# Performance work log

Hardware: AMD Instinct MI355X
Metric: run time of the kernel (lower is better)

Reference implementation:

```python
import jax, jax.numpy as jnp
import numpy as np

SOFTCAP = 50.0
EPS = 1e-6
N_HEADS, D_HEAD = 16, 64


def _rms(x, w):
    return x * jax.lax.rsqrt(jnp.mean(x * x, axis=-1, keepdims=True) + EPS) * w


def _rope(x, cos, sin):
    # Faithful to source: apply_rope uses x.size(1) as the position axis, but is
    # called on (B, H, T, Dh) tensors, so positions are indexed by HEAD index.
    n = x.shape[1]
    x1, x2 = x[..., 0::2], x[..., 1::2]
    c = cos[:n][None, :, None, :]
    s = sin[:n][None, :, None, :]
    return jnp.stack([x1 * c - x2 * s, x1 * s + x2 * c], axis=-1).reshape(x.shape)


def setup_inputs() -> dict:
    key = jax.random.key(0)
    ks = jax.random.split(key, 12)
    L, D, H, Dh, Dff, V, B, T = 6, 1024, N_HEADS, D_HEAD, 4096, 32000, 1, 1024
    r = lambda k, shape: jax.random.normal(k, shape, dtype=jnp.float32) * 0.02
    return {
        'x': jax.random.randint(ks[0], (B, T), 0, V, dtype=jnp.int32),
        'embed': r(ks[1], (V, D)),
        'ln1': jnp.ones((L, D), jnp.float32),
        'Wq': r(ks[2], (L, H * Dh, D)),
        'Wk': r(ks[3], (L, H * Dh, D)),
        'Wv': r(ks[4], (L, H * Dh, D)),
        'Wo': r(ks[5], (L, D, H * Dh)),
        'qn': jnp.ones((L, Dh), jnp.float32),
        'kn': jnp.ones((L, Dh), jnp.float32),
        'ln2': jnp.ones((L, D), jnp.float32),
        'Wg': r(ks[6], (L, Dff, D)),
        'Wu': r(ks[7], (L, Dff, D)),
        'Wd': r(ks[8], (L, D, Dff)),
        'ln_out': jnp.ones((D,), jnp.float32),
    }


def reference(x, embed, ln1, Wq, Wk, Wv, Wo, qn, kn, ln2, Wg, Wu, Wd, ln_out):
    B, T = x.shape
    H, Dh = N_HEADS, D_HEAD
    scale = Dh ** -0.5
    # RoPE tables (theta=10000)
    freqs = 1.0 / (10000.0 ** (jnp.arange(0, Dh, 2, dtype=jnp.float32) / Dh))
    ang = jnp.arange(T, dtype=jnp.float32)[:, None] * freqs[None, :]
    cos, sin = jnp.cos(ang), jnp.sin(ang)
    mask = jnp.triu(jnp.ones((T, T), dtype=bool), k=1)  # True above diagonal

    h = embed[x]  # (B, T, D)

    def block(h, p):
        l1, wq, wk, wv, wo, qnw, knw, l2, wg, wu, wd = p
        hn = _rms(h, l1)
        q = (hn @ wq.T).reshape(B, T, H, Dh).transpose(0, 2, 1, 3)  # (B,H,T,Dh)
        k = (hn @ wk.T).reshape(B, T, H, Dh).transpose(0, 2, 1, 3)
        v = (hn @ wv.T).reshape(B, T, H, Dh).transpose(0, 2, 1, 3)
        q = _rope(_rms(q, qnw), cos, sin)
        k = _rope(_rms(k, knw), cos, sin)
        scores = jnp.einsum('bhtd,bhsd->bhts', q, k) * scale
        scores = SOFTCAP * jnp.tanh(scores / SOFTCAP)
        scores = jnp.where(mask[None, None], -jnp.inf, scores)
        attn = jax.nn.softmax(scores, axis=-1)
        o = jnp.einsum('bhts,bhsd->bhtd', attn, v)
        o = o.transpose(0, 2, 1, 3).reshape(B, T, H * Dh)
        h = h + o @ wo.T
        hn2 = _rms(h, l2)
        h = h + (jax.nn.silu(hn2 @ wg.T) * (hn2 @ wu.T)) @ wd.T
        return h, None

    h, _ = jax.lax.scan(block, h, (ln1, Wq, Wk, Wv, Wo, qn, kn, ln2, Wg, Wu, Wd))
    # tied embed/head
    logits = _rms(h, ln_out) @ embed.T  # (B, T, V)
    return logits
```

## Files before the change

kernel.cpp:

```cpp
#include <hip/hip_runtime.h>
#include <math.h>
#include <type_traits>

typedef __bf16 bf16_t;
typedef bf16_t bf16x4 __attribute__((ext_vector_type(4)));
typedef bf16_t bf16x8 __attribute__((ext_vector_type(8)));
typedef float  f32x4  __attribute__((ext_vector_type(4)));

#define RMS_EPS 1e-6f

enum { EP_STORE = 0, EP_RESID = 1, EP_SPLIT = 2, EP_SILU = 3, EP_QKV = 4 };

template<int V> using IC = std::integral_constant<int, V>;

static __device__ __forceinline__ f32x4 mfma16(bf16x8 a, bf16x8 b, f32x4 c) {
    return __builtin_amdgcn_mfma_f32_16x16x32_bf16(a, b, c, 0, 0, 0);
}

#define GLDS(gp, lp) __builtin_amdgcn_global_load_lds( \
    (const __attribute__((address_space(1))) void*)(gp), \
    (__attribute__((address_space(3))) void*)(lp), 16, 0, 0)

template<int N> static __device__ __forceinline__ void vmwait() {
    if constexpr (N == 0)      asm volatile("s_waitcnt vmcnt(0)" ::: "memory");
    else if constexpr (N == 2) asm volatile("s_waitcnt vmcnt(2)" ::: "memory");
    else if constexpr (N == 3) asm volatile("s_waitcnt vmcnt(3)" ::: "memory");
    else if constexpr (N == 4) asm volatile("s_waitcnt vmcnt(4)" ::: "memory");
    else if constexpr (N == 6) asm volatile("s_waitcnt vmcnt(6)" ::: "memory");
    else if constexpr (N == 8) asm volatile("s_waitcnt vmcnt(8)" ::: "memory");
    __builtin_amdgcn_sched_barrier(0);
}
static __device__ __forceinline__ void bar() { __builtin_amdgcn_s_barrier(); }
static __device__ __forceinline__ void lgkm0() {
    asm volatile("s_waitcnt lgkmcnt(0)" ::: "memory");
    __builtin_amdgcn_sched_barrier(0);
}

template<int BM, int BN, int WR, int WC, int PLANES, int EPIL, int MINW, int DEPTH>
__global__ __launch_bounds__(WR * WC * 64, MINW)
void gemm_bf16(const bf16_t* __restrict__ Ah, const bf16_t* __restrict__ Al,
               const bf16_t* __restrict__ Bh,
               float* __restrict__ Cf, bf16_t* __restrict__ Ch, bf16_t* __restrict__ Cl,
               int K, int lda, int ldb, int ldc, long long sC,
               const float* __restrict__ qnw, const float* __restrict__ knw)
{
    constexpr int ASZ = BM * 32, BSZ = BN * 32;
    constexpr int NW = WR * WC;
    constexpr int NLD = (BM / 16 * (PLANES >= 2 ? 2 : 1) + BN / 16) / NW;
    __shared__ __align__(16) bf16_t sAh[DEPTH][ASZ], sBh[DEPTH][BSZ];
    __shared__ __align__(16) bf16_t sAl[PLANES >= 2 ? DEPTH : 1][PLANES >= 2 ? ASZ : 8];

    const int gx = gridDim.x;
    int id = blockIdx.x + gx * blockIdx.y;
    if (gridDim.z == 1) {
        int nwg = gx * gridDim.y;
        int q = nwg >> 3, r = nwg & 7;
        int xcd = id & 7, ix = id >> 3;
        id = (xcd < r ? xcd * (q + 1) : r * (q + 1) + (xcd - r) * q) + ix;
    }
    const int bm = id % gx, bn = id / gx;
    const int row0 = bm * BM, col0 = bn * BN;

    const size_t kofs = (size_t)blockIdx.z * K;
    Ah += kofs;  Bh += kofs;
    if constexpr (PLANES >= 2) Al += kofs;

    const int tid = threadIdx.x, lane = tid & 63, wave = tid >> 6;
    const int lr = lane & 15, lg = lane >> 4;
    constexpr int WM = BM / WR, WN = BN / WC, MF = WM / 16, NF = WN / 16;
    const int wr = wave / WC, wc = wave % WC;

    f32x4 acc[MF][NF];
    #pragma unroll
    for (int m = 0; m < MF; ++m)
        #pragma unroll
        for (int n = 0; n < NF; ++n) acc[m][n] = (f32x4){0.f, 0.f, 0.f, 0.f};

    auto stage = [&](int k0, int p) {
        #pragma unroll
        for (int i = wave; i < BM / 16; i += NW) {
            int s = i * 64 + lane, rr = s >> 2, c = s & 3;
            size_t go = (size_t)(row0 + rr) * lda + k0 + ((c ^ ((rr >> 1) & 3)) << 3);
            GLDS(Ah + go, &sAh[p][i * 512]);
            if constexpr (PLANES >= 2) GLDS(Al + go, &sAl[p][i * 512]);
        }
        #pragma unroll
        for (int i = wave; i < BN / 16; i += NW) {
            int s = i * 64 + lane, rr = s >> 2, c = s & 3;
            size_t go = (size_t)(col0 + rr) * ldb + k0 + ((c ^ ((rr >> 1) & 3)) << 3);
            GLDS(Bh + go, &sBh[p][i * 512]);
        }
    };

    auto compute = [&](int p) {
        bf16x8 ahf[MF], alf[MF], bhf[NF];
        #pragma unroll
        for (int m = 0; m < MF; ++m) {
            int rr = wr * WM + m * 16 + lr;
            int by = rr * 64 + ((lg ^ ((rr >> 1) & 3)) << 4);
            ahf[m] = *(const bf16x8*)((const char*)&sAh[p][0] + by);
            if constexpr (PLANES >= 2)
                alf[m] = *(const bf16x8*)((const char*)&sAl[p][0] + by);
        }
        #pragma unroll
        for (int n = 0; n < NF; ++n) {
            int rr = wc * WN + n * 16 + lr;
            int by = rr * 64 + ((lg ^ ((rr >> 1) & 3)) << 4);
            bhf[n] = *(const bf16x8*)((const char*)&sBh[p][0] + by);
        }
        #pragma unroll
        for (int m = 0; m < MF; ++m)
            #pragma unroll
            for (int n = 0; n < NF; ++n) {
                acc[m][n] = mfma16(ahf[m], bhf[n], acc[m][n]);
                if constexpr (PLANES >= 2)
                    acc[m][n] = mfma16(alf[m], bhf[n], acc[m][n]);
            }
    };

    if constexpr (DEPTH == 3) {
        const int NC = K >> 5;
        stage(0, 0);
        stage(32, 1);
        for (int j = 0; j + 2 < NC; ++j) {
            stage(32 * (j + 2), (j + 2) % 3);
            vmwait<2 * NLD>(); bar();
            compute(j % 3);
            bar();
        }
        vmwait<NLD>(); bar();
        compute((K >> 5) >= 2 ? ((K >> 5) - 2) % 3 : 0);
        vmwait<0>(); bar();
        compute(((K >> 5) - 1) % 3);
    } else {
        stage(0, 0);
        int k0 = 32;
        for (; k0 + 32 < K; k0 += 64) {
            stage(k0, 1);
            vmwait<NLD>(); bar();
            compute(0);
            bar();
            stage(k0 + 32, 0);
            vmwait<NLD>(); bar();
            compute(1);
            bar();
        }
        stage(k0, 1);
        vmwait<NLD>(); bar();
        compute(0);
        bar();
        vmwait<0>(); bar();
        compute(1);
    }

    if constexpr (EPIL == EP_QKV) {
        const int colbase = col0 + wc * WN;
        const int typ = colbase >> 10;
        if (typ < 2) {
            const float* nw = (typ == 0) ? qnw : knw;
            const int hh = (colbase - typ * 1024) >> 6;
            constexpr float kLogF = -0.41524101186092029f;
            #pragma unroll
            for (int m = 0; m < MF; ++m)
                #pragma unroll
                for (int r = 0; r < 4; ++r) {
                    int grow = row0 + wr * WM + m * 16 + lg * 4 + r;
                    float ss = 0.f;
                    #pragma unroll
                    for (int n = 0; n < NF; ++n) {
                        float v = acc[m][n][r];
                        ss += v * v;
                    }
                    ss += __shfl_xor(ss, 1, 64);
                    ss += __shfl_xor(ss, 2, 64);
                    ss += __shfl_xor(ss, 4, 64);
                    ss += __shfl_xor(ss, 8, 64);
                    float inv = rsqrtf(ss * (1.0f / 64.0f) + RMS_EPS);
                    #pragma unroll
                    for (int n = 0; n < NF; ++n) {
                        int i = n * 16 + lr;
                        float x = acc[m][n][r] * inv * nw[i];
                        float p = __shfl_xor(x, 1, 64);
                        float f = exp2f((float)(i >> 1) * kLogF);
                        float ang = (float)hh * f;
                        float cs = cosf(ang), sn = sinf(ang);
                        float o = (lr & 1) ? (p * sn + x * cs) : (x * cs - p * sn);
                        Ch[(size_t)grow * ldc + colbase + i] = (bf16_t)o;
                    }
                }
        } else {
            bf16_t* vTh_ = Cl;
            bf16_t* vTl_ = (bf16_t*)Cf;
            const int vcb = colbase - 2048;
            #pragma unroll
            for (int m = 0; m < MF; ++m)
                #pragma unroll
                for (int n = 0; n < NF; ++n) {
                    int vc = vcb + n * 16 + lr;
                    int grow0 = row0 + wr * WM + m * 16 + lg * 4;
                    bf16x4 hv, lv;
                    #pragma unroll
                    for (int r = 0; r < 4; ++r) {
                        float v = acc[m][n][r];
                        bf16_t hb = (bf16_t)v;
                        hv[r] = hb;
                        lv[r] = (bf16_t)(v - (float)hb);
                    }
                    *(bf16x4*)&vTh_[(size_t)vc * 1024 + grow0] = hv;
                    *(bf16x4*)&vTl_[(size_t)vc * 1024 + grow0] = lv;
                }
        }
        return;
    }

    #pragma unroll
    for (int m = 0; m < MF; ++m)
        #pragma unroll
        for (int n = 0; n < NF; ++n)
            #pragma unroll
            for (int r = 0; r < 4; ++r) {
                int grow = row0 + wr * WM + m * 16 + lg * 4 + r;
                int gcol = col0 + wc * WN + n * 16 + lr;
                float v = acc[m][n][r];
                size_t off = (size_t)blockIdx.z * sC + (size_t)grow * ldc + gcol;
                if constexpr (EPIL == EP_STORE) {
                    Cf[off] = v;
                } else if constexpr (EPIL == EP_RESID) {
                    Cf[off] += v;
                } else if constexpr (EPIL == EP_SPLIT) {
                    bf16_t hb = (bf16_t)v;
                    Ch[off] = hb;
                    Cl[off] = (bf16_t)(v - (float)hb);
                }
            }
}

__global__ __launch_bounds__(512, 4)
void gemm_gu_pack(const bf16_t* __restrict__ Ah, const bf16_t* __restrict__ Bh,
                  bf16_t* __restrict__ Ch,
                  const float* wq, const float* wk, const float* wv,
                  const float* wo, const float* wg, const float* wu,
                  const float* wd, bf16_t* wAd, bf16_t* wGUd, bf16_t* wdd,
                  const float* __restrict__ embed, bf16_t* __restrict__ eh,
                  int es, int ee)
{
    constexpr int lda = 1024, ldb = 1024, ldc = 4096, K = 1024;
    const int tid = threadIdx.x;

    if (blockIdx.z == 2) {
        int base = ((int)blockIdx.y * 8 + (int)blockIdx.x) * 512 + tid;
        for (int j = 0; j < 11; ++j) {
            int u = es + j * 131072 + base;
            if (u < ee) {
                f32x4 v = ((const f32x4*)embed)[u];
                bf16x4 hv;
                #pragma unroll
                for (int q2 = 0; q2 < 4; ++q2) hv[q2] = (bf16_t)v[q2];
                ((bf16x4*)eh)[u] = hv;
            }
        }
        return;
    }

    if (blockIdx.z == 1) {
        if (!wq) return;
        int base = ((int)blockIdx.y * 8 + (int)blockIdx.x) * 512 + tid;
        #pragma unroll 4
        for (int j = 0; j < 32; ++j) {
            int v = j * 131072 + base;
            f32x4 val;
            bf16_t* dst;
            size_t doff;
            if (v < (1 << 20)) {
                int b = v >> 8, col = v & 255;
                const float* src = b < 1024 ? wq : b < 2048 ? wk : b < 3072 ? wv : wo;
                val = ((const f32x4*)src)[(size_t)(b & 1023) * 256 + col];
                dst = wAd; doff = (size_t)b * 256 + col;
            } else if (v < 3 * (1 << 20)) {
                int u = v - (1 << 20);
                int bb = u >> 8, col = u & 255;
                int row = bb < 4096 ? 2 * bb : 2 * (bb - 4096) + 1;
                const float* src = bb < 4096 ? wg : wu;
                val = ((const f32x4*)src)[(size_t)(bb & 4095) * 256 + col];
                dst = wGUd; doff = (size_t)row * 256 + col;
            } else {
                int u = v - 3 * (1 << 20);
                val = ((const f32x4*)wd)[u];
                dst = wdd; doff = (size_t)u;
            }
            bf16x4 hv;
            #pragma unroll
            for (int q2 = 0; q2 < 4; ++q2) hv[q2] = (bf16_t)val[q2];
            ((bf16x4*)dst)[doff] = hv;
        }
        return;
    }

    __shared__ __align__(16) bf16_t sA[3][128 * 32], sB[3][256 * 32];

    int id = blockIdx.x + 8 * blockIdx.y;
    {
        int q = 256 >> 3;
        int xcd = id & 7, ix = id >> 3;
        id = xcd * q + ix;
    }
    const int bm = id % 8, bn = id / 8;
    const int row0 = bm * 128, col0 = bn * 256;

    const int lane = tid & 63, wave = tid >> 6;
    const int lr = lane & 15, lg = lane >> 4;
    const int wr = wave >> 2, wc = wave & 3;

    f32x4 acc[4][4];
    #pragma unroll
    for (int m = 0; m < 4; ++m)
        #pragma unroll
        for (int n = 0; n < 4; ++n) acc[m][n] = (f32x4){0.f, 0.f, 0.f, 0.f};

    auto stage = [&](int k0, int p) {
        {
            int i = wave;
            int s = i * 64 + lane, rr = s >> 2, c = s & 3;
            size_t go = (size_t)(row0 + rr) * lda + k0 + ((c ^ ((rr >> 1) & 3)) << 3);
            GLDS(Ah + go, &sA[p][i * 512]);
        }
        #pragma unroll
        for (int i = wave; i < 16; i += 8) {
            int s = i * 64 + lane, rr = s >> 2, c = s & 3;
            size_t go = (size_t)(col0 + rr) * ldb + k0 + ((c ^ ((rr >> 1) & 3)) << 3);
            GLDS(Bh + go, &sB[p][i * 512]);
        }
    };

    auto compute = [&](int p) {
        bf16x8 af[4], bf4[4];
        #pragma unroll
        for (int m = 0; m < 4; ++m) {
            int rr = wr * 64 + m * 16 + lr;
            int by = rr * 64 + ((lg ^ ((rr >> 1) & 3)) << 4);
            af[m] = *(const bf16x8*)((const char*)&sA[p][0] + by);
        }
        #pragma unroll
        for (int n = 0; n < 4; ++n) {
            int rr = wc * 64 + n * 16 + lr;
            int by = rr * 64 + ((lg ^ ((rr >> 1) & 3)) << 4);
            bf4[n] = *(const bf16x8*)((const char*)&sB[p][0] + by);
        }
        #pragma unroll
        for (int m = 0; m < 4; ++m)
            #pragma unroll
            for (int n = 0; n < 4; ++n)
                acc[m][n] = mfma16(af[m], bf4[n], acc[m][n]);
    };

    const int NC = K >> 5;
    stage(0, 0);
    stage(32, 1);
    for (int j = 0; j + 2 < NC; ++j) {
        stage(32 * (j + 2), (j + 2) % 3);
        vmwait<6>(); bar();
        compute(j % 3);
        bar();
    }
    vmwait<3>(); bar();
    compute((NC - 2) % 3);
    vmwait<0>(); bar();
    compute((NC - 1) % 3);

    #pragma unroll
    for (int m = 0; m < 4; ++m)
        #pragma unroll
        for (int n = 0; n < 4; ++n)
            #pragma unroll
            for (int r = 0; r < 4; ++r) {
                int grow = row0 + wr * 64 + m * 16 + lg * 4 + r;
                int gcol = col0 + wc * 64 + n * 16 + lr;
                float v = acc[m][n][r];
                float pv = __shfl_xor(v, 1, 64);
                if (!(lr & 1)) {
                    float s = (v / (1.0f + __expf(-v))) * pv;
                    Ch[(size_t)grow * ldc + (gcol >> 1)] = (bf16_t)s;
                }
            }
}

__global__ __launch_bounds__(512, 2)
void gemm_logits8(const bf16_t* __restrict__ Ah, const bf16_t* __restrict__ Bh,
                  float* __restrict__ Cf)
{
    constexpr int lda = 1024, ldb = 1024, ldc = 32000;
    constexpr int NT = 16;
    __shared__ __align__(16) bf16_t sA[2][2][256 * 32];
    __shared__ __align__(16) bf16_t sB[2][2][256 * 32];

    const int gx = gridDim.x;
    int id = blockIdx.x + gx * blockIdx.y;
    {
        int nwg = gx * gridDim.y;
        int q = nwg >> 3, r = nwg & 7;
        int xcd = id & 7, ix = id >> 3;
        id = (xcd < r ? xcd * (q + 1) : r * (q + 1) + (xcd - r) * q) + ix;
    }
    const int bm = id % gx, bn = id / gx;
    const int row0 = bm * 256, col0 = bn * 256;

    const int tid = threadIdx.x, lane = tid & 63, wave = tid >> 6;
    const int lr = lane & 15, lg = lane >> 4;
    const int wr = wave >> 2, wc = wave & 3;

    f32x4 acc[8][4];
    #pragma unroll
    for (int m = 0; m < 8; ++m)
        #pragma unroll
        for (int n = 0; n < 4; ++n) acc[m][n] = (f32x4){0.f, 0.f, 0.f, 0.f};

    auto stageA = [&](int chunk, int buf, int ks) {
        int k0 = chunk * 32;
        #pragma unroll
        for (int i = wave; i < 16; i += 8) {
            int s = i * 64 + lane, rr = s >> 2, c = s & 3;
            size_t go = (size_t)(row0 + rr) * lda + k0 + ((c ^ ((rr >> 1) & 3)) << 3);
            GLDS(Ah + go, &sA[buf][ks][i * 512]);
        }
    };
    auto stageB = [&](int chunk, int buf, int ks) {
        int k0 = chunk * 32;
        #pragma unroll
        for (int i = wave; i < 16; i += 8) {
            int s = i * 64 + lane, rr = s >> 2, c = s & 3;
            size_t go = (size_t)(col0 + rr) * ldb + k0 + ((c ^ ((rr >> 1) & 3)) << 3);
            GLDS(Bh + go, &sB[buf][ks][i * 512]);
        }
    };

    auto phase = [&](int t, auto ksc) {
        constexpr int ks = decltype(ksc)::value;
        const int buf = t & 1;
        bf16x8 af[8], bf4[4];
        #pragma unroll
        for (int m = 0; m < 8; ++m) {
            int rr = wr * 128 + m * 16 + lr;
            int by = rr * 64 + ((lg ^ ((rr >> 1) & 3)) << 4);
            af[m] = *(const bf16x8*)((const char*)&sA[buf][ks][0] + by);
        }
        #pragma unroll
        for (int n = 0; n < 4; ++n) {
            int rr = wc * 64 + n * 16 + lr;
            int by = rr * 64 + ((lg ^ ((rr >> 1) & 3)) << 4);
            bf4[n] = *(const bf16x8*)((const char*)&sB[buf][ks][0] + by);
        }
        if constexpr (ks == 0) {
            if (t + 1 < NT) {
                stageA(2 * (t + 1) + 1, (t + 1) & 1, 1);
                stageB(2 * (t + 1) + 1, (t + 1) & 1, 1);
                vmwait<8>();
            } else {
                vmwait<0>();
            }
        } else {
            if (t + 2 < NT) {
                stageA(2 * (t + 2), t & 1, 0);
                stageB(2 * (t + 2), t & 1, 0);
                vmwait<8>();
            } else if (t + 1 < NT) {
                vmwait<4>();
            } else {
                vmwait<0>();
            }
        }
        bar();
        lgkm0();
        __builtin_amdgcn_s_setprio(1);
        #pragma unroll
        for (int m = 0; m < 8; ++m)
            #pragma unroll
            for (int n = 0; n < 4; ++n)
                acc[m][n] = mfma16(af[m], bf4[n], acc[m][n]);
        __builtin_amdgcn_s_setprio(0);
        bar();
    };

    stageA(0, 0, 0); stageB(0, 0, 0);
    stageA(1, 0, 1); stageB(1, 0, 1);
    stageA(2, 1, 0); stageB(2, 1, 0);
    vmwait<8>(); bar();

    for (int t = 0; t < NT; ++t) {
        phase(t, IC<0>{});
        phase(t, IC<1>{});
    }

    #pragma unroll
    for (int m = 0; m < 8; ++m)
        #pragma unroll
        for (int n = 0; n < 4; ++n)
            #pragma unroll
            for (int r = 0; r < 4; ++r) {
                int grow = row0 + wr * 128 + m * 16 + lg * 4 + r;
                int gcol = col0 + wc * 64 + n * 16 + lr;
                Cf[(size_t)grow * ldc + gcol] = acc[m][n][r];
            }
}

static __device__ __forceinline__ void wsplit_body(
    int b2, int tid,
    const float* wq, const float* wk, const float* wv, const float* wo,
    const float* wg, const float* wu, const float* wd,
    bf16_t* wAh, bf16_t* wGUh, bf16_t* wdh)
{
    #pragma unroll
    for (int k = 0; k < 4; ++k) {
        int b = b2 * 4 + k;
        const float* src;
        bf16_t* dst;
        size_t so, doff;
        if (b < 4096) {
            src = b < 1024 ? wq : b < 2048 ? wk : b < 3072 ? wv : wo;
            so = (size_t)(b & 1023) * 256 + tid;
            doff = (size_t)b * 256 + tid;
            dst = wAh;
        } else if (b < 12288) {
            int bb = b - 4096;
            int row = bb < 4096 ? 2 * bb : 2 * (bb - 4096) + 1;
            src = bb < 4096 ? wg : wu;
            so = (size_t)(bb & 4095) * 256 + tid;
            doff = (size_t)row * 256 + tid;
            dst = wGUh;
        } else {
            src = wd;
            so = (size_t)(b - 12288) * 256 + tid;
            doff = so;
            dst = wdh;
        }
        f32x4 v = ((const f32x4*)src)[so];
        bf16x4 hv;
        #pragma unroll
        for (int j = 0; j < 4; ++j) hv[j] = (bf16_t)v[j];
        ((bf16x4*)dst)[doff] = hv;
    }
}

__global__ __launch_bounds__(256)
void reduce_rms(const float* __restrict__ p, float* __restrict__ h,
                const float* __restrict__ w, bf16_t* __restrict__ outh)
{
    int blk = blockIdx.x, tid = threadIdx.x;
    size_t i = (size_t)blk * 256 + tid;
    const size_t S = (1024 * 1024) / 4;
    f32x4 a = ((const f32x4*)p)[i];
    f32x4 b = ((const f32x4*)p)[i + S];
    f32x4 c = ((const f32x4*)p)[i + 2 * S];
    f32x4 d = ((const f32x4*)p)[i + 3 * S];
    f32x4 hv = ((const f32x4*)h)[i];
    #pragma unroll
    for (int j = 0; j < 4; ++j) hv[j] += (a[j] + b[j]) + (c[j] + d[j]);
    ((f32x4*)h)[i] = hv;

    float ss = hv[0]*hv[0] + hv[1]*hv[1] + hv[2]*hv[2] + hv[3]*hv[3];
    #pragma unroll
    for (int m = 1; m < 64; m <<= 1) ss += __shfl_xor(ss, m, 64);
    __shared__ float red[4];
    if ((tid & 63) == 0) red[tid >> 6] = ss;
    __syncthreads();
    float tot = red[0] + red[1] + red[2] + red[3];
    float inv = rsqrtf(tot * (1.0f / 1024.0f) + RMS_EPS);
    f32x4 wt4 = *(const f32x4*)(w + tid * 4);
    bf16x4 hv4;
    #pragma unroll
    for (int j = 0; j < 4; ++j) hv4[j] = (bf16_t)(hv[j] * inv * wt4[j]);
    ((bf16x4*)outh)[i] = hv4;
}

__global__ __launch_bounds__(256)
void gather_rms_wsplit(const int* __restrict__ ids, const float* __restrict__ embed,
                       const float* __restrict__ w, float* __restrict__ h,
                       bf16_t* __restrict__ outh,
                       const float* wq, const float* wk, const float* wv,
                       const float* wo, const float* wg, const float* wu,
                       const float* wd, bf16_t* wAh, bf16_t* wGUh, bf16_t* wdh)
{
    int blk = blockIdx.x, tid = threadIdx.x;
    if (blk >= 1024) {
        wsplit_body(blk - 1024, tid, wq, wk, wv, wo, wg, wu, wd, wAh, wGUh, wdh);
        return;
    }
    int row = ids[blk];
    f32x4 v = ((const f32x4*)(embed + (size_t)row * 1024))[tid];
    ((f32x4*)(h + (size_t)blk * 1024))[tid] = v;

    float ss = v[0]*v[0] + v[1]*v[1] + v[2]*v[2] + v[3]*v[3];
    #pragma unroll
    for (int m = 1; m < 64; m <<= 1) ss += __shfl_xor(ss, m, 64);
    __shared__ float red[4];
    if ((tid & 63) == 0) red[tid >> 6] = ss;
    __syncthreads();
    float tot = red[0] + red[1] + red[2] + red[3];
    float inv = rsqrtf(tot * (1.0f / 1024.0f) + RMS_EPS);
    f32x4 wt4 = *(const f32x4*)(w + tid * 4);
    bf16x4 hv;
    #pragma unroll
    for (int j = 0; j < 4; ++j) hv[j] = (bf16_t)(v[j] * inv * wt4[j]);
    ((bf16x4*)outh)[(size_t)blk * 256 + tid] = hv;
}

__global__ __launch_bounds__(128, 2)
void flash_attn(const bf16_t* __restrict__ qkvh,
                const bf16_t* __restrict__ vTh, const bf16_t* __restrict__ vTl,
                bf16_t* __restrict__ oh)
{
    __shared__ __align__(16) bf16_t sQ[32*64], sK[64*64], sVh[64*64], sVl[64*64];
    __shared__ __align__(16) bf16_t sPh[32*64], sPl[32*64];

    const int q0 = blockIdx.x * 32;
    const int hh = blockIdx.y;
    const int tid = threadIdx.x, lane = tid & 63, w = tid >> 6;
    const int lr = lane & 15, lg = lane >> 4;

    #pragma unroll
    for (int ii = 0; ii < 2; ++ii) {
        int r0 = w * 16 + ii * 8;
        int r  = r0 + (lane >> 3);
        int i  = lane & 7;
        GLDS(qkvh + (size_t)(q0 + r) * 3072 + hh * 64 + ((i ^ (r & 7)) << 3),
             sQ + r0 * 64);
    }
    __syncthreads();

    bf16x8 qa[2];
    #pragma unroll
    for (int ks = 0; ks < 2; ++ks) {
        int r = w * 16 + lr;
        qa[ks] = *(const bf16x8*)((const char*)sQ + r * 128 +
                                  ((((ks << 2) | lg) ^ (r & 7)) << 4));
    }

    f32x4 o_acc[4];
    #pragma unroll
    for (int n = 0; n < 4; ++n) o_acc[n] = (f32x4){0.f, 0.f, 0.f, 0.f};
    float m_run[4] = {-1e30f, -1e30f, -1e30f, -1e30f};
    float l_run[4] = {0.f, 0.f, 0.f, 0.f};

    const int ntiles = ((q0 + 31) >> 6) + 1;
    for (int t = 0; t < ntiles; ++t) {
        const int kv0 = t * 64;
        #pragma unroll
        for (int ii = 0; ii < 4; ++ii) {
            int r0 = w * 32 + ii * 8;
            int r  = r0 + (lane >> 3);
            int i  = lane & 7;
            GLDS(qkvh + (size_t)(kv0 + r) * 3072 + 1024 + hh * 64 + ((i ^ (r & 7)) << 3),
                 sK + r0 * 64);
            GLDS(vTh + (size_t)(hh * 64 + r) * 1024 + kv0 + ((i ^ (r & 7)) << 3),
                 sVh + r0 * 64);
            GLDS(vTl + (size_t)(hh * 64 + r) * 1024 + kv0 + ((i ^ (r & 7)) << 3),
                 sVl + r0 * 64);
        }
        __syncthreads();

        f32x4 s_acc[4];
        #pragma unroll
        for (int n = 0; n < 4; ++n) s_acc[n] = (f32x4){0.f, 0.f, 0.f, 0.f};
        #pragma unroll
        for (int ks = 0; ks < 2; ++ks)
            #pragma unroll
            for (int n = 0; n < 4; ++n) {
                int r = n * 16 + lr;
                bf16x8 kb = *(const bf16x8*)((const char*)sK + r * 128 +
                                             ((((ks << 2) | lg) ^ (r & 7)) << 4));
                s_acc[n] = mfma16(qa[ks], kb, s_acc[n]);
            }

        #pragma unroll
        for (int j = 0; j < 4; ++j) {
            int qr = q0 + w * 16 + lg * 4 + j;
            float p[4];
            float mx = -1e30f;
            #pragma unroll
            for (int n = 0; n < 4; ++n) {
                float sx = s_acc[n][j] * (0.125f * 0.02f);
                float v = 50.f * (1.f - 2.f / (1.f + __expf(2.f * sx)));
                int key = kv0 + n * 16 + lr;
                if (key > qr) v = -1e30f;
                p[n] = v;
                mx = fmaxf(mx, v);
            }
            #pragma unroll
            for (int m = 1; m < 16; m <<= 1) mx = fmaxf(mx, __shfl_xor(mx, m, 64));
            float mn = fmaxf(m_run[j], mx);
            float ef = __expf(m_run[j] - mn);
            m_run[j] = mn;
            float rs = 0.f;
            #pragma unroll
            for (int n = 0; n < 4; ++n) {
                float e = __expf(p[n] - mn);
                p[n] = e;
                rs += e;
            }
            #pragma unroll
            for (int m = 1; m < 16; m <<= 1) rs += __shfl_xor(rs, m, 64);
            l_run[j] = l_run[j] * ef + rs;
            #pragma unroll
            for (int n = 0; n < 4; ++n) o_acc[n][j] *= ef;
            int r = w * 16 + lg * 4 + j;
            #pragma unroll
            for (int n = 0; n < 4; ++n) {
                int c = n * 16 + lr;
                int byo = r * 128 + ((((c >> 3) ^ (r & 7)) << 4)) + ((c & 7) << 1);
                bf16_t hb = (bf16_t)p[n];
                *(bf16_t*)((char*)sPh + byo) = hb;
                *(bf16_t*)((char*)sPl + byo) = (bf16_t)(p[n] - (float)hb);
            }
        }

        #pragma unroll
        for (int ks = 0; ks < 2; ++ks) {
            int pr = w * 16 + lr;
            int pby = pr * 128 + ((((ks << 2) | lg) ^ (pr & 7)) << 4);
            bf16x8 pa  = *(const bf16x8*)((const char*)sPh + pby);
            bf16x8 pl_ = *(const bf16x8*)((const char*)sPl + pby);
            #pragma unroll
            for (int n = 0; n < 4; ++n) {
                int vr = n * 16 + lr;
                int vby = vr * 128 + ((((ks << 2) | lg) ^ (vr & 7)) << 4);
                bf16x8 vhf = *(const bf16x8*)((const char*)sVh + vby);
                bf16x8 vlf = *(const bf16x8*)((const char*)sVl + vby);
                o_acc[n] = mfma16(pa,  vhf, o_acc[n]);
                o_acc[n] = mfma16(pl_, vhf, o_acc[n]);
                o_acc[n] = mfma16(pa,  vlf, o_acc[n]);
            }
        }
        __syncthreads();
    }

    #pragma unroll
    for (int j = 0; j < 4; ++j) {
        float inv = 1.0f / l_run[j];
        int qr = q0 + w * 16 + lg * 4 + j;
        #pragma unroll
        for (int n = 0; n < 4; ++n) {
            size_t off = (size_t)qr * 1024 + hh * 64 + n * 16 + lr;
            oh[off] = (bf16_t)(o_acc[n][j] * inv);
        }
    }
}

__global__ __launch_bounds__(256)
void rmsnorm_split(const float* __restrict__ in, const float* __restrict__ w,
                   bf16_t* __restrict__ outh)
{
    int row = blockIdx.x, tid = threadIdx.x;
    f32x4 v = *(const f32x4*)(in + (size_t)row * 1024 + tid * 4);
    float ss = v[0]*v[0] + v[1]*v[1] + v[2]*v[2] + v[3]*v[3];
    #pragma unroll
    for (int m = 1; m < 64; m <<= 1) ss += __shfl_xor(ss, m, 64);
    __shared__ float red[4];
    if ((tid & 63) == 0) red[tid >> 6] = ss;
    __syncthreads();
    float tot = red[0] + red[1] + red[2] + red[3];
    float inv = rsqrtf(tot * (1.0f / 1024.0f) + RMS_EPS);
    f32x4 wt4 = *(const f32x4*)(w + tid * 4);
    bf16x4 hv;
    #pragma unroll
    for (int j = 0; j < 4; ++j) hv[j] = (bf16_t)(v[j] * inv * wt4[j]);
    ((bf16x4*)outh)[(size_t)row * 256 + tid] = hv;
}

extern "C" void kernel_launch(void* const* d_in, const int* in_sizes, int n_in,
                              void* d_out, int out_size, void* d_ws, size_t ws_size,
                              hipStream_t stream)
{
    (void)in_sizes; (void)n_in; (void)out_size; (void)ws_size;
    const int*   x_ids = (const int*)  d_in[0];
    const float* embed = (const float*)d_in[1];
    const float* ln1   = (const float*)d_in[2];
    const float* Wq    = (const float*)d_in[3];
    const float* Wk    = (const float*)d_in[4];
    const float* Wv    = (const float*)d_in[5];
    const float* Wo    = (const float*)d_in[6];
    const float* qn    = (const float*)d_in[7];
    const float* kn    = (const float*)d_in[8];
    const float* ln2   = (const float*)d_in[9];
    const float* Wg    = (const float*)d_in[10];
    const float* Wu    = (const float*)d_in[11];
    const float* Wd    = (const float*)d_in[12];
    const float* lnout = (const float*)d_in[13];
    float* out = (float*)d_out;

    char* ws = (char*)d_ws;
    const size_t MB = 1 << 20;
    float*  h    = (float*) (ws +   0 * MB);
    bf16_t* hnh  = (bf16_t*)(ws +   4 * MB);
    bf16_t* qkvh = (bf16_t*)(ws +   8 * MB);
    bf16_t* vTh  = (bf16_t*)(ws +  20 * MB);
    bf16_t* vTl  = (bf16_t*)(ws +  22 * MB);
    bf16_t* oh   = (bf16_t*)(ws +  24 * MB);
    bf16_t* wA[2]  = {(bf16_t*)(ws +  28 * MB), (bf16_t*)(ws +  84 * MB)};
    bf16_t* wGU[2] = {(bf16_t*)(ws +  36 * MB), (bf16_t*)(ws +  92 * MB)};
    bf16_t* wD[2]  = {(bf16_t*)(ws +  52 * MB), (bf16_t*)(ws + 108 * MB)};
    bf16_t* silh = (bf16_t*)(ws +  60 * MB);
    float*  wdp  = (float*) (ws +  68 * MB);
    bf16_t* eh   = (bf16_t*)(ws + 116 * MB);

    const long long M1 = 1024 * 1024;
    const int ETOT = 8192000;
    const int ESL  = 1365334;

    gather_rms_wsplit<<<5120, 256, 0, stream>>>(
        x_ids, embed, ln1, h, hnh,
        Wq, Wk, Wv, Wo, Wg, Wu, Wd, wA[0], wGU[0], wD[0]);

    for (int l = 0; l < 6; ++l) {
        const int s = l & 1, nx = s ^ 1;

        gemm_bf16<64,128,2,2,1,EP_QKV,4,3><<<dim3(16,24),256,0,stream>>>(
            hnh, nullptr, wA[s], (float*)vTl, qkvh, vTh, 1024, 1024, 1024, 3072, 0,
            qn + l * 64, kn + l * 64);

        flash_attn<<<dim3(32,16), 128, 0, stream>>>(qkvh, vTh, vTl, oh);

        gemm_bf16<64,64,2,2,1,EP_RESID,4,3><<<dim3(16,16),256,0,stream>>>(
            oh, nullptr, wA[s] + 3 * M1, h, nullptr, nullptr, 1024, 1024, 1024, 1024, 0,
            nullptr, nullptr);

        rmsnorm_split<<<1024, 256, 0, stream>>>(h, ln2 + l * 1024, hnh);

        int es = l * ESL, ee = (l + 1) * ESL < ETOT ? (l + 1) * ESL : ETOT;
        gemm_gu_pack<<<dim3(8,32,3), 512, 0, stream>>>(
            hnh, wGU[s], silh,
            l < 5 ? Wq + (size_t)(l+1) * M1 : nullptr,
            l < 5 ? Wk + (size_t)(l+1) * M1 : nullptr,
            l < 5 ? Wv + (size_t)(l+1) * M1 : nullptr,
            l < 5 ? Wo + (size_t)(l+1) * M1 : nullptr,
            l < 5 ? Wg + (size_t)(l+1) * 4 * M1 : nullptr,
            l < 5 ? Wu + (size_t)(l+1) * 4 * M1 : nullptr,
            l < 5 ? Wd + (size_t)(l+1) * 4 * M1 : nullptr,
            wA[nx], wGU[nx], wD[nx],
            embed, eh, es, ee);

        gemm_bf16<128,128,2,2,1,EP_STORE,4,3><<<dim3(8,8,4),256,0,stream>>>(
            silh, nullptr, wD[s], wdp, nullptr, nullptr, 1024, 4096, 4096, 1024, M1,
            nullptr, nullptr);

        const float* wnext = (l < 5) ? (ln1 + (l + 1) * 1024) : lnout;
        reduce_rms<<<1024, 256, 0, stream>>>(wdp, h, wnext, hnh);
    }

    gemm_logits8<<<dim3(4,125), 512, 0, stream>>>(hnh, eh, out);
}
```

Before: 1.095 ms.

## Double-buffer K/V tiles in flash attention and precompute RoPE tables

Flash attention now stages the next K/V tile into a second LDS buffer while the current tile is being computed. Partial vmcnt waits let the compute overlap with the global-to-LDS loads instead of stalling on a full sync every tile. Separately, the RoPE cos/sin values are computed once into small tables by an extra block of the setup kernel, so the QKV GEMM epilogue reads them instead of evaluating exp2/cos/sin per element. This costs double the K/V LDS footprint, which may reduce occupancy, plus a small table read per element.

```diff
diff --git a/kernel.cpp b/kernel.cpp
--- a/kernel.cpp
+++ b/kernel.cpp
@@ -22,12 +22,13 @@
     (__attribute__((address_space(3))) void*)(lp), 16, 0, 0)
 
 template<int N> static __device__ __forceinline__ void vmwait() {
-    if constexpr (N == 0)      asm volatile("s_waitcnt vmcnt(0)" ::: "memory");
-    else if constexpr (N == 2) asm volatile("s_waitcnt vmcnt(2)" ::: "memory");
-    else if constexpr (N == 3) asm volatile("s_waitcnt vmcnt(3)" ::: "memory");
-    else if constexpr (N == 4) asm volatile("s_waitcnt vmcnt(4)" ::: "memory");
-    else if constexpr (N == 6) asm volatile("s_waitcnt vmcnt(6)" ::: "memory");
-    else if constexpr (N == 8) asm volatile("s_waitcnt vmcnt(8)" ::: "memory");
+    if constexpr (N == 0)       asm volatile("s_waitcnt vmcnt(0)" ::: "memory");
+    else if constexpr (N == 2)  asm volatile("s_waitcnt vmcnt(2)" ::: "memory");
+    else if constexpr (N == 3)  asm volatile("s_waitcnt vmcnt(3)" ::: "memory");
+    else if constexpr (N == 4)  asm volatile("s_waitcnt vmcnt(4)" ::: "memory");
+    else if constexpr (N == 6)  asm volatile("s_waitcnt vmcnt(6)" ::: "memory");
+    else if constexpr (N == 8)  asm volatile("s_waitcnt vmcnt(8)" ::: "memory");
+    else if constexpr (N == 12) asm volatile("s_waitcnt vmcnt(12)" ::: "memory");
     __builtin_amdgcn_sched_barrier(0);
 }
 static __device__ __forceinline__ void bar() { __builtin_amdgcn_s_barrier(); }
@@ -42,7 +43,8 @@
                const bf16_t* __restrict__ Bh,
                float* __restrict__ Cf, bf16_t* __restrict__ Ch, bf16_t* __restrict__ Cl,
                int K, int lda, int ldb, int ldc, long long sC,
-               const float* __restrict__ qnw, const float* __restrict__ knw)
+               const float* __restrict__ qnw, const float* __restrict__ knw,
+               const float* __restrict__ ctab, const float* __restrict__ stab)
 {
     constexpr int ASZ = BM * 32, BSZ = BN * 32;
     constexpr int NW = WR * WC;
@@ -159,7 +161,6 @@
         if (typ < 2) {
             const float* nw = (typ == 0) ? qnw : knw;
             const int hh = (colbase - typ * 1024) >> 6;
-            constexpr float kLogF = -0.41524101186092029f;
             #pragma unroll
             for (int m = 0; m < MF; ++m)
                 #pragma unroll
@@ -181,9 +182,8 @@
                         int i = n * 16 + lr;
                         float x = acc[m][n][r] * inv * nw[i];
                         float p = __shfl_xor(x, 1, 64);
-                        float f = exp2f((float)(i >> 1) * kLogF);
-                        float ang = (float)hh * f;
-                        float cs = cosf(ang), sn = sinf(ang);
+                        float cs = ctab[(hh << 5) + (i >> 1)];
+                        float sn = stab[(hh << 5) + (i >> 1)];
                         float o = (lr & 1) ? (p * sn + x * cs) : (x * cs - p * sn);
                         Ch[(size_t)grow * ldc + colbase + i] = (bf16_t)o;
                     }
@@ -577,9 +577,21 @@
                        bf16_t* __restrict__ outh,
                        const float* wq, const float* wk, const float* wv,
                        const float* wo, const float* wg, const float* wu,
-                       const float* wd, bf16_t* wAh, bf16_t* wGUh, bf16_t* wdh)
+                       const float* wd, bf16_t* wAh, bf16_t* wGUh, bf16_t* wdh,
+                       float* __restrict__ ctab, float* __restrict__ stab)
 {
     int blk = blockIdx.x, tid = threadIdx.x;
+    if (blk == 5120) {
+        constexpr float kLogF = -0.41524101186092029f;
+        for (int e = tid; e < 512; e += 256) {
+            int hh = e >> 5, p0 = e & 31;
+            float f = exp2f((float)p0 * kLogF);
+            float ang = (float)hh * f;
+            ctab[e] = cosf(ang);
+            stab[e] = sinf(ang);
+        }
+        return;
+    }
     if (blk >= 1024) {
         wsplit_body(blk - 1024, tid, wq, wk, wv, wo, wg, wu, wd, wAh, wGUh, wdh);
         return;
@@ -608,7 +620,8 @@
                 const bf16_t* __restrict__ vTh, const bf16_t* __restrict__ vTl,
                 bf16_t* __restrict__ oh)
 {
-    __shared__ __align__(16) bf16_t sQ[32*64], sK[64*64], sVh[64*64], sVl[64*64];
+    __shared__ __align__(16) bf16_t sQ[32*64];
+    __shared__ __align__(16) bf16_t sK[2][64*64], sVh[2][64*64], sVl[2][64*64];
     __shared__ __align__(16) bf16_t sPh[32*64], sPl[32*64];
 
     const int q0 = blockIdx.x * 32;
@@ -624,24 +637,8 @@
         GLDS(qkvh + (size_t)(q0 + r) * 3072 + hh * 64 + ((i ^ (r & 7)) << 3),
              sQ + r0 * 64);
     }
-    __syncthreads();
-
-    bf16x8 qa[2];
-    #pragma unroll
-    for (int ks = 0; ks < 2; ++ks) {
-        int r = w * 16 + lr;
-        qa[ks] = *(const bf16x8*)((const char*)sQ + r * 128 +
-                                  ((((ks << 2) | lg) ^ (r & 7)) << 4));
-    }
-
-    f32x4 o_acc[4];
-    #pragma unroll
-    for (int n = 0; n < 4; ++n) o_acc[n] = (f32x4){0.f, 0.f, 0.f, 0.f};
-    float m_run[4] = {-1e30f, -1e30f, -1e30f, -1e30f};
-    float l_run[4] = {0.f, 0.f, 0.f, 0.f};
-
-    const int ntiles = ((q0 + 31) >> 6) + 1;
-    for (int t = 0; t < ntiles; ++t) {
+
+    auto stageKV = [&](int t, int buf) {
         const int kv0 = t * 64;
         #pragma unroll
         for (int ii = 0; ii < 4; ++ii) {
@@ -649,13 +646,42 @@
             int r  = r0 + (lane >> 3);
             int i  = lane & 7;
             GLDS(qkvh + (size_t)(kv0 + r) * 3072 + 1024 + hh * 64 + ((i ^ (r & 7)) << 3),
-                 sK + r0 * 64);
+                 sK[buf] + r0 * 64);
             GLDS(vTh + (size_t)(hh * 64 + r) * 1024 + kv0 + ((i ^ (r & 7)) << 3),
-                 sVh + r0 * 64);
+                 sVh[buf] + r0 * 64);
             GLDS(vTl + (size_t)(hh * 64 + r) * 1024 + kv0 + ((i ^ (r & 7)) << 3),
-                 sVl + r0 * 64);
-        }
-        __syncthreads();
+                 sVl[buf] + r0 * 64);
+        }
+    };
+
+    const int ntiles = ((q0 + 31) >> 6) + 1;
+    stageKV(0, 0);
+
+    bf16x8 qa[2];
+    f32x4 o_acc[4];
+    #pragma unroll
+    for (int n = 0; n < 4; ++n) o_acc[n] = (f32x4){0.f, 0.f, 0.f, 0.f};
+    float m_run[4] = {-1e30f, -1e30f, -1e30f, -1e30f};
+    float l_run[4] = {0.f, 0.f, 0.f, 0.f};
+
+    for (int t = 0; t < ntiles; ++t) {
+        const int kv0 = t * 64;
+        const int buf = t & 1;
+        if (t + 1 < ntiles) {
+            stageKV(t + 1, buf ^ 1);
+            vmwait<12>();
+        } else {
+            vmwait<0>();
+        }
+        bar();
+        if (t == 0) {
+            #pragma unroll
+            for (int ks = 0; ks < 2; ++ks) {
+                int r = w * 16 + lr;
+                qa[ks] = *(const bf16x8*)((const char*)sQ + r * 128 +
+                                          ((((ks << 2) | lg) ^ (r & 7)) << 4));
+            }
+        }
 
         f32x4 s_acc[4];
         #pragma unroll
@@ -665,7 +691,7 @@
             #pragma unroll
             for (int n = 0; n < 4; ++n) {
                 int r = n * 16 + lr;
-                bf16x8 kb = *(const bf16x8*)((const char*)sK + r * 128 +
+                bf16x8 kb = *(const bf16x8*)((const char*)&sK[buf][0] + r * 128 +
                                              ((((ks << 2) | lg) ^ (r & 7)) << 4));
                 s_acc[n] = mfma16(qa[ks], kb, s_acc[n]);
             }
@@ -722,14 +748,14 @@
             for (int n = 0; n < 4; ++n) {
                 int vr = n * 16 + lr;
                 int vby = vr * 128 + ((((ks << 2) | lg) ^ (vr & 7)) << 4);
-                bf16x8 vhf = *(const bf16x8*)((const char*)sVh + vby);
-                bf16x8 vlf = *(const bf16x8*)((const char*)sVl + vby);
+                bf16x8 vhf = *(const bf16x8*)((const char*)&sVh[buf][0] + vby);
+                bf16x8 vlf = *(const bf16x8*)((const char*)&sVl[buf][0] + vby);
                 o_acc[n] = mfma16(pa,  vhf, o_acc[n]);
                 o_acc[n] = mfma16(pl_, vhf, o_acc[n]);
                 o_acc[n] = mfma16(pa,  vlf, o_acc[n]);
             }
         }
-        __syncthreads();
+        bar();
     }
 
     #pragma unroll
@@ -800,27 +826,29 @@
     bf16_t* silh = (bf16_t*)(ws +  60 * MB);
     float*  wdp  = (float*) (ws +  68 * MB);
     bf16_t* eh   = (bf16_t*)(ws + 116 * MB);
+    float*  ctab = (float*) (ws + 179 * MB);
+    float*  stab = (float*) (ws + 179 * MB + 4096);
 
     const long long M1 = 1024 * 1024;
     const int ETOT = 8192000;
     const int ESL  = 1365334;
 
-    gather_rms_wsplit<<<5120, 256, 0, stream>>>(
+    gather_rms_wsplit<<<5121, 256, 0, stream>>>(
         x_ids, embed, ln1, h, hnh,
-        Wq, Wk, Wv, Wo, Wg, Wu, Wd, wA[0], wGU[0], wD[0]);
+        Wq, Wk, Wv, Wo, Wg, Wu, Wd, wA[0], wGU[0], wD[0], ctab, stab);
 
     for (int l = 0; l < 6; ++l) {
         const int s = l & 1, nx = s ^ 1;
 
         gemm_bf16<64,128,2,2,1,EP_QKV,4,3><<<dim3(16,24),256,0,stream>>>(
             hnh, nullptr, wA[s], (float*)vTl, qkvh, vTh, 1024, 1024, 1024, 3072, 0,
-            qn + l * 64, kn + l * 64);
+            qn + l * 64, kn + l * 64, ctab, stab);
 
         flash_attn<<<dim3(32,16), 128, 0, stream>>>(qkvh, vTh, vTl, oh);
 
         gemm_bf16<64,64,2,2,1,EP_RESID,4,3><<<dim3(16,16),256,0,stream>>>(
             oh, nullptr, wA[s] + 3 * M1, h, nullptr, nullptr, 1024, 1024, 1024, 1024, 0,
-            nullptr, nullptr);
+            nullptr, nullptr, nullptr, nullptr);
 
         rmsnorm_split<<<1024, 256, 0, stream>>>(h, ln2 + l * 1024, hnh);
 
@@ -839,7 +867,7 @@
 
         gemm_bf16<128,128,2,2,1,EP_STORE,4,3><<<dim3(8,8,4),256,0,stream>>>(
             silh, nullptr, wD[s], wdp, nullptr, nullptr, 1024, 4096, 4096, 1024, M1,
-            nullptr, nullptr);
+            nullptr, nullptr, nullptr, nullptr);
 
         const float* wnext = (l < 5) ? (ln1 + (l + 1) * 1024) : lnout;
         reduce_rms<<<1024, 256, 0, stream>>>(wdp, h, wnext, hnh);
```

New measurement: 1.040 ms. 5.0% less time.
